# Kernel tuning notes

Hardware: AMD Instinct MI355X
Metric: run time of the kernel (lower is better)

The kernel has to match this reference:

```python
import jax, jax.numpy as jnp
import numpy as np

E, D, I, TOPK, N = 8, 2048, 4096, 2, 4096


def setup_inputs() -> dict:
    key = jax.random.key(0)
    k_x, k_w, k_i, k_g, k_u, k_d = jax.random.split(key, 6)
    x = jax.random.normal(k_x, (N, D), dtype=jnp.float32)
    expert_weights = jax.random.uniform(k_w, (N, TOPK), dtype=jnp.float32)
    expert_indices = jax.random.randint(k_i, (N, TOPK), 0, E).astype(jnp.int32)
    s_in = np.float32(1.0 / np.sqrt(D))
    s_mid = np.float32(1.0 / np.sqrt(I))
    # SwitchLinear weights: [num_experts, out_features, in_features]
    wg = jax.random.normal(k_g, (E, I, D), dtype=jnp.float32) * s_in
    wu = jax.random.normal(k_u, (E, I, D), dtype=jnp.float32) * s_in
    wd = jax.random.normal(k_d, (E, D, I), dtype=jnp.float32) * s_mid
    return {"x": x, "expert_weights": expert_weights,
            "expert_indices": expert_indices, "top_k": TOPK,
            "wg": wg, "wu": wu, "wd": wd}


def reference(x, expert_weights, expert_indices, top_k, wg, wu, wd):
    # out[n] = sum_k expert_weights[n,k] * Wd[e] @ (silu(Wg[e] x[n]) * (Wu[e] x[n]))
    #          with e = expert_indices[n,k].
    # Grouped-by-expert form (identical math): accumulate each expert's
    # contribution over all tokens, weighted by its routing weight (0 if not routed).
    num_experts = wg.shape[0]
    out = jnp.zeros_like(x)
    for e in range(num_experts):
        # per-token routing weight for expert e (sums over top_k slots)
        w_e = jnp.sum(jnp.where(expert_indices == e, expert_weights, 0.0), axis=-1)  # [N]
        gate = x @ wg[e].T            # [N, I]
        up = x @ wu[e].T              # [N, I]
        h = jax.nn.silu(gate) * up    # SwiGLU, [N, I]
        out = out + w_e[:, None] * (h @ wd[e].T)  # [N, D]
    return out
```

## Files before the change

kernel.cpp:

```cpp
#include <hip/hip_runtime.h>
#include <hip/hip_bf16.h>
#include <math.h>

#define E_ 8
#define D_ 2048
#define I_ 4096
#define TOPK_ 2
#define N_ 4096
#define NPAIR (N_*TOPK_)
#define PADMAX 10240
#define MAXTB 40
#define CVTX 12
#define CH_X   (1L<<20)
#define CH_HALF (1L<<22)
#define CH_WD  (1L<<23)

typedef __attribute__((ext_vector_type(8))) short s8v;
typedef __attribute__((ext_vector_type(8))) unsigned short us8;
typedef __attribute__((ext_vector_type(4))) float f32x4;
typedef const __attribute__((address_space(1))) void* gvp;
typedef __attribute__((address_space(3))) void* lvp;

__device__ __forceinline__ unsigned short f2bf(float f) {
  union { float f; unsigned int u; } c; c.f = f;
  unsigned int u = c.u;
  u += 0x7fffu + ((u >> 16) & 1u);
  return (unsigned short)(u >> 16);
}

__device__ __forceinline__ void cvt_chunk(const float* __restrict__ src,
                                          unsigned short* __restrict__ dst,
                                          size_t off) {
  float4 a = *(const float4*)(src + off);
  float4 b = *(const float4*)(src + off + 4);
  us8 o;
  o[0]=f2bf(a.x); o[1]=f2bf(a.y); o[2]=f2bf(a.z); o[3]=f2bf(a.w);
  o[4]=f2bf(b.x); o[5]=f2bf(b.y); o[6]=f2bf(b.z); o[7]=f2bf(b.w);
  *(us8*)(dst + off) = o;
}

__device__ __forceinline__ void cvt_half(const float* __restrict__ src,
                                         unsigned short* __restrict__ dst,
                                         long chunk, int ihalf) {
  long f = chunk << 3;
  int e = (int)(f >> 22);
  long r = f & ((1L << 22) - 1);
  size_t off = ((size_t)e << 23) + ((size_t)ihalf << 22) + (size_t)r;
  cvt_chunk(src, dst, off);
}

__global__ __launch_bounds__(512)
void head_kernel(const int* __restrict__ idx, const float* __restrict__ ew,
                 int* cnt, int* offs, int* tb, int* ntb,
                 int* perm, float* wgt,
                 const float* __restrict__ x, unsigned short* __restrict__ xb,
                 const float* __restrict__ wg, unsigned short* __restrict__ wgb,
                 const float* __restrict__ wu, unsigned short* __restrict__ wub)
{
  if (blockIdx.x == 0) {
    __shared__ int scnt[E_], soff[E_ + 1], scur[E_];
    int t = threadIdx.x;
    if (t < E_) scnt[t] = 0;
    __syncthreads();
    for (int p = t; p < NPAIR; p += blockDim.x) atomicAdd(&scnt[idx[p]], 1);
    __syncthreads();
    if (t == 0) {
      int o = 0;
      for (int e = 0; e < E_; e++) {
        soff[e] = o; scur[e] = o;
        o += ((scnt[e] + 255) / 256) * 256;
      }
      soff[E_] = o;
      int T = 0;
      for (int e = 0; e < E_; e++) {
        int nb = (scnt[e] + 255) / 256;
        for (int rb = 0; rb < nb; rb++) tb[T++] = (e << 16) | rb;
      }
      *ntb = T;
      for (int e = 0; e < E_; e++) { cnt[e] = scnt[e]; offs[e] = soff[e]; }
      offs[E_] = o;
    }
    __syncthreads();
    for (int e = 0; e < E_; e++) {
      int start = soff[e] + scnt[e], end = soff[e + 1];
      for (int s = start + t; s < end; s += blockDim.x) { perm[s] = -1; wgt[s] = 0.f; }
    }
    __syncthreads();
    for (int p = t; p < NPAIR; p += blockDim.x) {
      int e = idx[p];
      int pos = atomicAdd(&scur[e], 1);
      perm[pos] = p / TOPK_;
      wgt[pos]  = ew[p];
    }
    return;
  }
  const long TOTAL = CH_X + 2 * CH_HALF;
  long c0 = (long)(blockIdx.x - 1) * 512 + threadIdx.x;
  long stride = (long)(gridDim.x - 1) * 512;
  for (long c = c0; c < TOTAL; c += stride) {
    if (c < CH_X) cvt_chunk(x, xb, (size_t)c << 3);
    else if (c < CH_X + CH_HALF) cvt_half(wg, wgb, c - CH_X, 0);
    else cvt_half(wu, wub, c - CH_X - CH_HALF, 0);
  }
}


#define SB  __builtin_amdgcn_sched_barrier(0)
#define BARR __builtin_amdgcn_s_barrier()
#define VMW(N) asm volatile("s_waitcnt vmcnt(" #N ")" ::: "memory")
#define PRIO1 __builtin_amdgcn_s_setprio(1)
#define PRIO0 __builtin_amdgcn_s_setprio(0)

#define STG(T,P) { \
  __builtin_amdgcn_global_load_lds((gvp)(aptr + (size_t)(T)*32), (lvp)(&smem[(P)*8192 + w*512]), 16, 0, 0); \
  __builtin_amdgcn_global_load_lds((gvp)(bptr + (size_t)(T)*32), (lvp)(&smem[16384 + (P)*8192 + w*512]), 16, 0, 0); }

#define TILE32(T,P,NT_) { \
  if ((T) == (NT_)-1) { VMW(0); } else { VMW(2); } \
  SB; BARR; SB; \
  { const unsigned short* ap_ = &smem[(P)*8192 + aOff]; \
    const unsigned short* bp_ = &smem[16384 + (P)*8192 + bOff]; \
    s8v af[4], bf[4]; \
    af[0]=*(const s8v*)(ap_);      af[1]=*(const s8v*)(ap_+512); \
    af[2]=*(const s8v*)(ap_+1024); af[3]=*(const s8v*)(ap_+1536); \
    bf[0]=*(const s8v*)(bp_);      bf[1]=*(const s8v*)(bp_+512); \
    bf[2]=*(const s8v*)(bp_+1024); bf[3]=*(const s8v*)(bp_+1536); \
    PRIO1; \
    _Pragma("unroll") for (int m_=0;m_<4;m_++) \
      _Pragma("unroll") for (int n_=0;n_<4;n_++) \
        acc[m_][n_] = __builtin_amdgcn_mfma_f32_16x16x32_bf16(af[m_], bf[n_], acc[m_][n_], 0,0,0); \
    PRIO0; } \
  SB; BARR; SB; \
  if ((T)+2 < (NT_)) { STG((T)+2, P); } }

#define KLOOP32(NT_) { \
  STG(0,0); STG(1,1); \
  _Pragma("unroll 1") for (int tt=0; tt<(NT_)/2; ++tt) { \
    TILE32(2*tt,   0, NT_); \
    TILE32(2*tt+1, 1, NT_); } }

__global__ __launch_bounds__(1024, 4)
void gu32_kernel(const unsigned short* __restrict__ xb,
                 const unsigned short* __restrict__ wgb,
                 const unsigned short* __restrict__ wub,
                 const int* __restrict__ tb, const int* __restrict__ ntb,
                 const int* __restrict__ offs, const int* __restrict__ perm,
                 unsigned short* __restrict__ H,
                 int i_base, int cvt_mode,
                 const float* __restrict__ cs0, unsigned short* __restrict__ cd0,
                 const float* __restrict__ cs1, unsigned short* __restrict__ cd1)
{
  __shared__ unsigned short smem[32768];

  int tid = threadIdx.x;
  if (blockIdx.x >= MAXTB) {
    long cid = (long)(blockIdx.x - MAXTB) + (long)CVTX * blockIdx.y;
    long c0 = cid * 1024 + tid;
    long stride = (long)CVTX * 16 * 1024;
    if (cvt_mode == 1) {
      for (long c = c0; c < 2 * CH_HALF; c += stride) {
        if (c < CH_HALF) cvt_half(cs0, cd0, c, 1);
        else cvt_half(cs1, cd1, c - CH_HALF, 1);
      }
    } else if (cvt_mode == 2) {
      for (long c = c0; c < CH_WD; c += stride) cvt_chunk(cs0, cd0, (size_t)c << 3);
    }
    return;
  }

  int lid = blockIdx.y * MAXTB + blockIdx.x;
  int sid = (lid & 7) * (MAXTB * 16 / 8) + (lid >> 3);
  int bx = sid % MAXTB;
  int by = sid / MAXTB;
  if (bx >= *ntb) return;
  int ent = tb[bx];
  int e = ent >> 16, rb = ent & 0xffff;
  int slotbase = offs[e] + rb * 256;
  int i0 = i_base + by * 128;

  int lane = tid & 63, w = tid >> 6;
  int wr = w >> 2, wc = w & 3;

  int cS = (lane & 7) ^ (lane >> 3);
  int rrS = 2 * (lane >> 3) + (cS >> 2);
  int kcS = (cS & 3) * 8;
  int tok = perm[slotbase + w * 16 + rrS]; if (tok < 0) tok = 0;
  const unsigned short* aptr = xb + (size_t)tok * D_ + kcS;
  const unsigned short* bptr = ((w & 1) ? wub : wgb)
      + ((size_t)e * I_ + i0 + (w >> 1) * 16 + rrS) * D_ + kcS;

  int hl = (lane & 15) >> 1;
  int pA = (((lane & 1) * 4 + (lane >> 4)) ^ hl) * 8;
  int aOff = wr * 2048 + hl * 64 + pA;
  int bOff = wc * 2048 + hl * 64 + pA;

  f32x4 acc[4][4];
#pragma unroll
  for (int m = 0; m < 4; m++)
#pragma unroll
    for (int n = 0; n < 4; n++) acc[m][n] = f32x4{0.f,0.f,0.f,0.f};

  KLOOP32(64);

#pragma unroll
  for (int m = 0; m < 4; m++) {
#pragma unroll
    for (int r = 0; r < 4; r++) {
      int row = wr * 64 + m * 16 + (lane >> 4) * 4 + r;
      size_t hbase = (size_t)(slotbase + row) * I_ + i0 + (lane & 15);
#pragma unroll
      for (int pr = 0; pr < 2; pr++) {
        float g = acc[m][pr*2][r];
        float u = acc[m][pr*2+1][r];
        float h = (g / (1.0f + __expf(-g))) * u;
        H[hbase + (2 * wc + pr) * 16] = f2bf(h);
      }
    }
  }
}

__global__ __launch_bounds__(1024, 4)
void down32_kernel(const unsigned short* __restrict__ H,
                   const unsigned short* __restrict__ wdb,
                   const int* __restrict__ tb, const int* __restrict__ ntb,
                   const int* __restrict__ offs, const int* __restrict__ perm,
                   const float* __restrict__ wgt,
                   float* __restrict__ out)
{
  __shared__ unsigned short smem[32768];

  int tid = threadIdx.x;
  int lid = (blockIdx.z * gridDim.y + blockIdx.y) * gridDim.x + blockIdx.x;
  int sid = (lid & 7) * 80 + (lid >> 3);
  int bx = sid % MAXTB;
  int rem = sid / MAXTB;
  int by = rem & 7;
  int z  = rem >> 3;
  if (bx >= *ntb) return;
  int ent = tb[bx];
  int e = ent >> 16, rb = ent & 0xffff;
  int slotbase = offs[e] + rb * 256;
  int d0 = by * 256;
  int kb = z * (I_ / 2);

  int lane = tid & 63, w = tid >> 6;
  int wr = w >> 2, wc = w & 3;

  int cS = (lane & 7) ^ (lane >> 3);
  int rrS = 2 * (lane >> 3) + (cS >> 2);
  int kcS = (cS & 3) * 8;
  const unsigned short* aptr = H + (size_t)(slotbase + w * 16 + rrS) * I_ + kcS + kb;
  const unsigned short* bptr = wdb + ((size_t)e * D_ + d0 + w * 16 + rrS) * I_ + kcS + kb;

  int hl = (lane & 15) >> 1;
  int pA = (((lane & 1) * 4 + (lane >> 4)) ^ hl) * 8;
  int aOff = wr * 2048 + hl * 64 + pA;
  int bOff = wc * 2048 + hl * 64 + pA;

  f32x4 acc[4][4];
#pragma unroll
  for (int m = 0; m < 4; m++)
#pragma unroll
    for (int n = 0; n < 4; n++) acc[m][n] = f32x4{0.f,0.f,0.f,0.f};

  KLOOP32(64);

#pragma unroll
  for (int m = 0; m < 4; m++) {
#pragma unroll
    for (int r = 0; r < 4; r++) {
      int row = wr * 64 + m * 16 + (lane >> 4) * 4 + r;
      int s = slotbase + row;
      int tok = perm[s];
      if (tok < 0) continue;
      float wv = wgt[s];
      float* op = out + (size_t)tok * D_ + d0 + wc * 64 + (lane & 15);
#pragma unroll
      for (int n = 0; n < 4; n++)
        atomicAdd(op + n * 16, acc[m][n][r] * wv);
    }
  }
}

extern "C" void kernel_launch(void* const* d_in, const int* in_sizes, int n_in,
                              void* d_out, int out_size, void* d_ws, size_t ws_size,
                              hipStream_t stream)
{
  const float* x  = (const float*)d_in[0];
  const float* ew = (const float*)d_in[1];
  const int*  idx = (const int*)d_in[2];
  const float* wg = (const float*)d_in[4];
  const float* wu = (const float*)d_in[5];
  const float* wd = (const float*)d_in[6];
  float* out = (float*)d_out;

  char* ws = (char*)d_ws;
  int* cnt   = (int*)(ws);
  int* ntb   = (int*)(ws + 64);
  int* tb    = (int*)(ws + 128);
  int* offs  = (int*)(ws + 640);
  int* perm  = (int*)(ws + 4096);
  float* wgt = (float*)(ws + 4096 + PADMAX * 4);

  const size_t xb_off = 131072;
  const size_t xb_b   = (size_t)N_ * D_ * 2;
  const size_t H_b    = (size_t)PADMAX * I_ * 2;
  const size_t w_b    = (size_t)E_ * I_ * D_ * 2;
  unsigned short* xb  = (unsigned short*)(ws + xb_off);
  unsigned short* H   = (unsigned short*)(ws + xb_off + xb_b);
  unsigned short* wgb = (unsigned short*)(ws + xb_off + xb_b + H_b);
  unsigned short* wub = (unsigned short*)((char*)wgb + w_b);
  unsigned short* wdb = (unsigned short*)((char*)wub + w_b);

  hipMemsetAsync(d_out, 0, (size_t)N_ * D_ * sizeof(float), stream);
  head_kernel<<<2048, 512, 0, stream>>>(idx, ew, cnt, offs, tb, ntb, perm, wgt,
                                        x, xb, wg, wgb, wu, wub);
  gu32_kernel<<<dim3(MAXTB + CVTX, 16), 1024, 0, stream>>>(
      xb, wgb, wub, tb, ntb, offs, perm, H, 0, 1, wg, wgb, wu, wub);
  gu32_kernel<<<dim3(MAXTB + CVTX, 16), 1024, 0, stream>>>(
      xb, wgb, wub, tb, ntb, offs, perm, H, I_ / 2, 2, wd, wdb,
      (const float*)0, (unsigned short*)0);
  down32_kernel<<<dim3(MAXTB, 8, 2), 1024, 0, stream>>>(
      H, wdb, tb, ntb, offs, perm, wgt, out);
}
```

Baseline: 804.9 us.

## Rebalance weight conversion across three gate/up launches and split down K four ways

```diff
diff --git a/kernel.cpp b/kernel.cpp
--- a/kernel.cpp
+++ b/kernel.cpp
@@ -10,10 +10,9 @@
 #define NPAIR (N_*TOPK_)
 #define PADMAX 10240
 #define MAXTB 40
-#define CVTX 12
+#define CVTX 24
 #define CH_X   (1L<<20)
 #define CH_HALF (1L<<22)
-#define CH_WD  (1L<<23)
 
 typedef __attribute__((ext_vector_type(8))) short s8v;
 typedef __attribute__((ext_vector_type(8))) unsigned short us8;
@@ -146,9 +145,13 @@
                  const int* __restrict__ tb, const int* __restrict__ ntb,
                  const int* __restrict__ offs, const int* __restrict__ perm,
                  unsigned short* __restrict__ H,
-                 int i_base, int cvt_mode,
-                 const float* __restrict__ cs0, unsigned short* __restrict__ cd0,
-                 const float* __restrict__ cs1, unsigned short* __restrict__ cd1)
+                 int by_base,
+                 const float* __restrict__ js1, unsigned short* __restrict__ jd1,
+                 long j1base, long j1tot,
+                 const float* __restrict__ js2, unsigned short* __restrict__ jd2,
+                 long j2base, long j2tot,
+                 const float* __restrict__ js3, unsigned short* __restrict__ jd3,
+                 long j3lo, long j3n)
 {
   __shared__ unsigned short smem[32768];
 
@@ -156,27 +159,35 @@
   if (blockIdx.x >= MAXTB) {
     long cid = (long)(blockIdx.x - MAXTB) + (long)CVTX * blockIdx.y;
     long c0 = cid * 1024 + tid;
-    long stride = (long)CVTX * 16 * 1024;
-    if (cvt_mode == 1) {
-      for (long c = c0; c < 2 * CH_HALF; c += stride) {
-        if (c < CH_HALF) cvt_half(cs0, cd0, c, 1);
-        else cvt_half(cs1, cd1, c - CH_HALF, 1);
+    long stride = (long)CVTX * gridDim.y * 1024;
+    long tot = j1tot + j2tot + j3n;
+    for (long c = c0; c < tot; c += stride) {
+      if (c < j1tot) {
+        long e = c >> 18, r = c & ((1L << 18) - 1);
+        cvt_chunk(js1, jd1, (size_t)(j1base + (e << 20) + r) << 3);
+      } else {
+        long c2 = c - j1tot;
+        if (c2 < j2tot) {
+          long e = c2 >> 18, r = c2 & ((1L << 18) - 1);
+          cvt_chunk(js2, jd2, (size_t)(j2base + (e << 20) + r) << 3);
+        } else {
+          cvt_chunk(js3, jd3, (size_t)(j3lo + (c2 - j2tot)) << 3);
+        }
       }
-    } else if (cvt_mode == 2) {
-      for (long c = c0; c < CH_WD; c += stride) cvt_chunk(cs0, cd0, (size_t)c << 3);
     }
     return;
   }
 
   int lid = blockIdx.y * MAXTB + blockIdx.x;
-  int sid = (lid & 7) * (MAXTB * 16 / 8) + (lid >> 3);
+  int cpx = (MAXTB * gridDim.y) >> 3;
+  int sid = (lid & 7) * cpx + (lid >> 3);
   int bx = sid % MAXTB;
-  int by = sid / MAXTB;
+  int by = by_base + sid / MAXTB;
   if (bx >= *ntb) return;
   int ent = tb[bx];
   int e = ent >> 16, rb = ent & 0xffff;
   int slotbase = offs[e] + rb * 256;
-  int i0 = i_base + by * 128;
+  int i0 = by * 128;
 
   int lane = tid & 63, w = tid >> 6;
   int wr = w >> 2, wc = w & 3;
@@ -231,7 +242,7 @@
 
   int tid = threadIdx.x;
   int lid = (blockIdx.z * gridDim.y + blockIdx.y) * gridDim.x + blockIdx.x;
-  int sid = (lid & 7) * 80 + (lid >> 3);
+  int sid = (lid & 7) * 160 + (lid >> 3);
   int bx = sid % MAXTB;
   int rem = sid / MAXTB;
   int by = rem & 7;
@@ -241,7 +252,7 @@
   int e = ent >> 16, rb = ent & 0xffff;
   int slotbase = offs[e] + rb * 256;
   int d0 = by * 256;
-  int kb = z * (I_ / 2);
+  int kb = z * (I_ / 4);
 
   int lane = tid & 63, w = tid >> 6;
   int wr = w >> 2, wc = w & 3;
@@ -263,7 +274,7 @@
 #pragma unroll
     for (int n = 0; n < 4; n++) acc[m][n] = f32x4{0.f,0.f,0.f,0.f};
 
-  KLOOP32(64);
+  KLOOP32(32);
 
 #pragma unroll
   for (int m = 0; m < 4; m++) {
@@ -312,14 +323,25 @@
   unsigned short* wub = (unsigned short*)((char*)wgb + w_b);
   unsigned short* wdb = (unsigned short*)((char*)wub + w_b);
 
+  const long P1BASE = 524288;
+  const long P2BASE = 786432;
+  const long PTOT   = 1L << 21;
+  const long WDQ    = 1L << 21;
+
   hipMemsetAsync(d_out, 0, (size_t)N_ * D_ * sizeof(float), stream);
   head_kernel<<<2048, 512, 0, stream>>>(idx, ew, cnt, offs, tb, ntb, perm, wgt,
                                         x, xb, wg, wgb, wu, wub);
-  gu32_kernel<<<dim3(MAXTB + CVTX, 16), 1024, 0, stream>>>(
-      xb, wgb, wub, tb, ntb, offs, perm, H, 0, 1, wg, wgb, wu, wub);
-  gu32_kernel<<<dim3(MAXTB + CVTX, 16), 1024, 0, stream>>>(
-      xb, wgb, wub, tb, ntb, offs, perm, H, I_ / 2, 2, wd, wdb,
-      (const float*)0, (unsigned short*)0);
-  down32_kernel<<<dim3(MAXTB, 8, 2), 1024, 0, stream>>>(
+  gu32_kernel<<<dim3(MAXTB + CVTX, 11), 1024, 0, stream>>>(
+      xb, wgb, wub, tb, ntb, offs, perm, H, 0,
+      wg, wgb, P1BASE, PTOT, wu, wub, P1BASE, PTOT, wd, wdb, 0, WDQ);
+  gu32_kernel<<<dim3(MAXTB + CVTX, 11), 1024, 0, stream>>>(
+      xb, wgb, wub, tb, ntb, offs, perm, H, 11,
+      wg, wgb, P2BASE, PTOT, wu, wub, P2BASE, PTOT, wd, wdb, WDQ, WDQ);
+  gu32_kernel<<<dim3(MAXTB + CVTX, 10), 1024, 0, stream>>>(
+      xb, wgb, wub, tb, ntb, offs, perm, H, 22,
+      (const float*)0, (unsigned short*)0, 0, 0,
+      (const float*)0, (unsigned short*)0, 0, 0,
+      wd, wdb, 2 * WDQ, 2 * WDQ);
+  down32_kernel<<<dim3(MAXTB, 8, 4), 1024, 0, stream>>>(
       H, wdb, tb, ntb, offs, perm, wgt, out);
 }
```

Result: slower. 1.019 ms (+26.6%).
